# Kernel tuning notes

Measured on AMD Instinct MI355X. Metric: run time of the kernel, lower is better.

## Reference

```python
import jax, jax.numpy as jnp
import numpy as np

B, T, N, D, H = 16, 96, 325, 64, 64
BS = 1e-09  # bias init constant

def _xavier(key, shape):
    fan_in, fan_out = shape
    limit = float(np.sqrt(6.0 / (fan_in + fan_out)))
    return jax.random.uniform(key, shape, jnp.float32, -limit, limit)

def setup_inputs() -> dict:
    key = jax.random.key(0)
    k = jax.random.split(key, 6)
    return {
        "x": jax.random.normal(k[0], (B, T, N, D), jnp.float32),
        "o_s": jax.random.normal(k[1], (B, T, N, D), jnp.float32),
        "U_x": _xavier(k[2], (D, 4 * H)),
        "V_x": _xavier(k[3], (H, 4 * H)),
        "b_x": jnp.full((4 * H,), BS, jnp.float32),
        "U_g": _xavier(k[4], (D, 2 * H)),
        "V_g": _xavier(k[5], (H, 2 * H)),
        "b_g": jnp.full((2 * H,), BS, jnp.float32),
    }

def reference(x, o_s, U_x, V_x, b_x, U_g, V_g, b_g):
    b, t, n, d = x.shape
    h = V_x.shape[0]
    ht0 = jnp.zeros((b, n, h), x.dtype)
    ct0 = jnp.zeros((b, n, h), x.dtype)

    def step(carry, inp):
        ht, ct = carry
        xt, ost = inp  # [b, n, d] each
        gates = xt @ U_x + ht @ V_x + b_x          # [b, n, 4h]
        gov = jax.nn.sigmoid(ost @ U_g + ht @ V_g + b_g)  # [b, n, 2h]
        ft = jax.nn.sigmoid(gates[..., :h])
        it = jax.nn.sigmoid(gates[..., h:2 * h])
        ot = jax.nn.sigmoid(gates[..., 2 * h:3 * h])
        ut = jax.nn.sigmoid(gates[..., 3 * h:])
        gov_f = gov[..., :h]
        gov_u = gov[..., h:]
        ct = gov_f * ft * ct + gov_u * it * ut
        ht = ot * jnp.tanh(ct)
        return (ht, ct), ht

    xs = (jnp.swapaxes(x, 0, 1), jnp.swapaxes(o_s, 0, 1))  # time-major [t, b, n, d]
    (ht, ct), hseq = jax.lax.scan(step, (ht0, ct0), xs)
    hidden_seq = jnp.swapaxes(hseq, 0, 1)  # [b, t, n, h]
    return hidden_seq, ht, ct
```

## Files before the change

### kernel.cpp

```cpp
#include <hip/hip_runtime.h>
#include <stdint.h>


#define TT 96
#define NNROW 325
#define STEP_OFS 20800
#define HT_OFS 31948800
#define CT_OFS 32281600

typedef __attribute__((ext_vector_type(8))) short short8;
typedef __attribute__((ext_vector_type(4))) short short4v;
typedef __attribute__((ext_vector_type(4))) float f32x4;

#define A_STRIDE 200
#define G_STRIDE 20

#define BAR() asm volatile("s_waitcnt lgkmcnt(0)\n\ts_barrier" ::: "memory")

__device__ __forceinline__ short f2bf(float f) {
    union { float f; uint32_t u; } v; v.f = f;
    uint32_t r = (v.u + 0x7FFFu + ((v.u >> 16) & 1u)) >> 16;
    return (short)(r & 0xFFFFu);
}
__device__ __forceinline__ float frcp(float x) { return __builtin_amdgcn_rcpf(x); }
__device__ __forceinline__ float fsig(float x) { return frcp(1.0f + __expf(-x)); }
__device__ __forceinline__ float ftanh_fast(float x) {
    return 1.0f - 2.0f * frcp(__expf(2.0f * x) + 1.0f);
}

__global__ __launch_bounds__(256, 2)
void glstm_kernel(const float* __restrict__ x,
                  const float* __restrict__ o_s,
                  const float* __restrict__ U_x,
                  const float* __restrict__ V_x,
                  const float* __restrict__ b_x,
                  const float* __restrict__ U_g,
                  const float* __restrict__ V_g,
                  const float* __restrict__ b_g,
                  float* __restrict__ out)
{
    __shared__ __align__(16) short Abuf[16 * A_STRIDE];
    __shared__ __align__(16) float Gbuf[384 * G_STRIDE];

    const int tid  = threadIdx.x;
    const int g    = blockIdx.x;
    const int lane = tid & 63;
    const int w    = tid >> 6;
    const int q    = lane >> 4;
    const int ln   = lane & 15;

    short8 frW[4][4];
    short8 frG[2][4];
    #pragma unroll
    for (int nt = 0; nt < 4; ++nt) {
        const int col = w * 64 + nt * 16 + ln;
        #pragma unroll
        for (int kb = 0; kb < 4; ++kb) {
            const float* Wp = (kb < 2) ? (U_x + (size_t)(kb * 32 + q * 8) * 256 + col)
                                       : (V_x + (size_t)((kb - 2) * 32 + q * 8) * 256 + col);
            short8 fr;
            #pragma unroll
            for (int j = 0; j < 8; ++j) fr[j] = f2bf(Wp[(size_t)j * 256]);
            frW[nt][kb] = fr;
        }
    }
    #pragma unroll
    for (int nt = 0; nt < 2; ++nt) {
        const int col = w * 32 + nt * 16 + ln;
        #pragma unroll
        for (int kb = 0; kb < 4; ++kb) {
            const float* Wp = (kb < 2) ? (U_g + (size_t)(kb * 32 + q * 8) * 128 + col)
                                       : (V_g + (size_t)((kb - 2) * 32 + q * 8) * 128 + col);
            short8 fr;
            #pragma unroll
            for (int j = 0; j < 8; ++j) fr[j] = f2bf(Wp[(size_t)j * 128]);
            frG[nt][kb] = fr;
        }
    }

    const int sm = tid >> 4;
    const int sd = tid & 15;
    const int srow = g * 16 + sm;
    const int sb = srow / NNROW;
    const int sn = srow - sb * NNROW;
    const size_t sbase = ((size_t)(sb * TT) * NNROW + sn) * 64 + sd * 4;

    const int hcol = tid & 63;
    const int rg   = tid >> 6;
    float ct[4] = {0.f, 0.f, 0.f, 0.f};
    const float bf_ = b_x[hcol];
    const float bi_ = b_x[64 + hcol];
    const float bo_ = b_x[128 + hcol];
    const float bu_ = b_x[192 + hcol];
    const float bgf = b_g[hcol];
    const float bgu = b_g[64 + hcol];
    size_t obase[4];
    int    fo[4];
    #pragma unroll
    for (int e = 0; e < 4; ++e) {
        const int m = rg * 4 + e;
        const int row = g * 16 + m;
        const int b = row / NNROW;
        const int n = row - b * NNROW;
        obase[e] = ((size_t)(b * TT) * NNROW + n) * 64 + hcol;
        fo[e]    = (b * NNROW + n) * 64 + hcol;
    }

    {
        short4v z = {0, 0, 0, 0};
        *(short4v*)&Abuf[sm * A_STRIDE + 128 + sd * 4] = z;
    }

    float4 xqA = *(const float4*)(x   + sbase);
    float4 oqA = *(const float4*)(o_s + sbase);
    float4 xqB = *(const float4*)(x   + sbase + (size_t)STEP_OFS);
    float4 oqB = *(const float4*)(o_s + sbase + (size_t)STEP_OFS);

    auto step = [&](int t, float4& xq, float4& oq) {
        {
            short4v sx = { f2bf(xq.x), f2bf(xq.y), f2bf(xq.z), f2bf(xq.w) };
            short4v so = { f2bf(oq.x), f2bf(oq.y), f2bf(oq.z), f2bf(oq.w) };
            *(short4v*)&Abuf[sm * A_STRIDE + sd * 4]      = sx;
            *(short4v*)&Abuf[sm * A_STRIDE + 64 + sd * 4] = so;
        }
        {
            int tn = t + 2; if (tn > TT - 1) tn = TT - 1;
            xq = *(const float4*)(x   + sbase + (size_t)tn * STEP_OFS);
            oq = *(const float4*)(o_s + sbase + (size_t)tn * STEP_OFS);
        }
        BAR();

        {
            const short* Ab = &Abuf[ln * A_STRIDE + q * 8];
            const short8 ax0 = *(const short8*)(Ab + 0);
            const short8 ax1 = *(const short8*)(Ab + 32);
            const short8 ao0 = *(const short8*)(Ab + 64);
            const short8 ao1 = *(const short8*)(Ab + 96);
            const short8 ah0 = *(const short8*)(Ab + 128);
            const short8 ah1 = *(const short8*)(Ab + 160);
            #pragma unroll
            for (int nt = 0; nt < 4; ++nt) {
                f32x4 acc = {0.f, 0.f, 0.f, 0.f};
                acc = __builtin_amdgcn_mfma_f32_16x16x32_bf16(ax0, frW[nt][0], acc, 0, 0, 0);
                acc = __builtin_amdgcn_mfma_f32_16x16x32_bf16(ax1, frW[nt][1], acc, 0, 0, 0);
                acc = __builtin_amdgcn_mfma_f32_16x16x32_bf16(ah0, frW[nt][2], acc, 0, 0, 0);
                acc = __builtin_amdgcn_mfma_f32_16x16x32_bf16(ah1, frW[nt][3], acc, 0, 0, 0);
                const int col = w * 64 + nt * 16 + ln;
                *(f32x4*)&Gbuf[col * G_STRIDE + q * 4] = acc;
            }
            #pragma unroll
            for (int nt = 0; nt < 2; ++nt) {
                f32x4 acc = {0.f, 0.f, 0.f, 0.f};
                acc = __builtin_amdgcn_mfma_f32_16x16x32_bf16(ao0, frG[nt][0], acc, 0, 0, 0);
                acc = __builtin_amdgcn_mfma_f32_16x16x32_bf16(ao1, frG[nt][1], acc, 0, 0, 0);
                acc = __builtin_amdgcn_mfma_f32_16x16x32_bf16(ah0, frG[nt][2], acc, 0, 0, 0);
                acc = __builtin_amdgcn_mfma_f32_16x16x32_bf16(ah1, frG[nt][3], acc, 0, 0, 0);
                const int col = 256 + w * 32 + nt * 16 + ln;
                *(f32x4*)&Gbuf[col * G_STRIDE + q * 4] = acc;
            }
        }
        BAR();

        {
            const f32x4 vf = *(const f32x4*)&Gbuf[(hcol      ) * G_STRIDE + rg * 4];
            const f32x4 vi = *(const f32x4*)&Gbuf[( 64 + hcol) * G_STRIDE + rg * 4];
            const f32x4 vo = *(const f32x4*)&Gbuf[(128 + hcol) * G_STRIDE + rg * 4];
            const f32x4 vu = *(const f32x4*)&Gbuf[(192 + hcol) * G_STRIDE + rg * 4];
            const f32x4 vgf = *(const f32x4*)&Gbuf[(256 + hcol) * G_STRIDE + rg * 4];
            const f32x4 vgu = *(const f32x4*)&Gbuf[(320 + hcol) * G_STRIDE + rg * 4];
            const size_t tofs = (size_t)t * STEP_OFS;
            #pragma unroll
            for (int e = 0; e < 4; ++e) {
                const int m = rg * 4 + e;
                float c = fsig(vgf[e] + bgf) * fsig(vf[e] + bf_) * ct[e]
                        + fsig(vgu[e] + bgu) * fsig(vi[e] + bi_) * fsig(vu[e] + bu_);
                ct[e] = c;
                float h = fsig(vo[e] + bo_) * ftanh_fast(c);
                out[obase[e] + tofs] = h;
                Abuf[m * A_STRIDE + 128 + hcol] = f2bf(h);
                if (t == TT - 1) {
                    out[HT_OFS + fo[e]] = h;
                    out[CT_OFS + fo[e]] = c;
                }
            }
        }
    };

    for (int t = 0; t < TT; t += 2) {
        step(t,     xqA, oqA);
        step(t + 1, xqB, oqB);
    }
}

extern "C" void kernel_launch(void* const* d_in, const int* in_sizes, int n_in,
                              void* d_out, int out_size, void* d_ws, size_t ws_size,
                              hipStream_t stream) {
    const float* x   = (const float*)d_in[0];
    const float* o_s = (const float*)d_in[1];
    const float* U_x = (const float*)d_in[2];
    const float* V_x = (const float*)d_in[3];
    const float* b_x = (const float*)d_in[4];
    const float* V_g = (const float*)d_in[6];
    const float* U_g = (const float*)d_in[5];
    const float* b_g = (const float*)d_in[7];
    float* out = (float*)d_out;

    glstm_kernel<<<dim3(325), dim3(256), 0, stream>>>(x, o_s, U_x, V_x, b_x, U_g, V_g, b_g, out);
}
```

Baseline: 366.4 us.

## Remap MFMA gate tiles per wave to drop LDS gate exchange and barrier

Each wave now computes the f/i/o/u and gov gate tiles for the same 16 hidden channels, so the pointwise LSTM update runs directly on the MFMA accumulators. The Gbuf round-trip and one of the two barriers per timestep go away. X/O/H staging becomes double-buffered, XOR-swizzled LDS tiles, and the prefetch distance grows by one step. The activations are rewritten with exp2 and shared reciprocals, and bf16 conversion uses v_cvt_pk_bf16_f32, which may shift rounding and numerics slightly.

```diff
diff --git a/kernel.cpp b/kernel.cpp
--- a/kernel.cpp
+++ b/kernel.cpp
@@ -9,11 +9,7 @@
 #define CT_OFS 32281600
 
 typedef __attribute__((ext_vector_type(8))) short short8;
-typedef __attribute__((ext_vector_type(4))) short short4v;
 typedef __attribute__((ext_vector_type(4))) float f32x4;
-
-#define A_STRIDE 200
-#define G_STRIDE 20
 
 #define BAR() asm volatile("s_waitcnt lgkmcnt(0)\n\ts_barrier" ::: "memory")
 
@@ -23,9 +19,11 @@
     return (short)(r & 0xFFFFu);
 }
 __device__ __forceinline__ float frcp(float x) { return __builtin_amdgcn_rcpf(x); }
-__device__ __forceinline__ float fsig(float x) { return frcp(1.0f + __expf(-x)); }
-__device__ __forceinline__ float ftanh_fast(float x) {
-    return 1.0f - 2.0f * frcp(__expf(2.0f * x) + 1.0f);
+__device__ __forceinline__ float ex2(float x)  { return __builtin_amdgcn_exp2f(x); }
+__device__ __forceinline__ uint32_t cvtpk(float lo, float hi) {
+    uint32_t r;
+    asm("v_cvt_pk_bf16_f32 %0, %1, %2" : "=v"(r) : "v"(lo), "v"(hi));
+    return r;
 }
 
 __global__ __launch_bounds__(256, 2)
@@ -39,8 +37,9 @@
                   const float* __restrict__ b_g,
                   float* __restrict__ out)
 {
-    __shared__ __align__(16) short Abuf[16 * A_STRIDE];
-    __shared__ __align__(16) float Gbuf[384 * G_STRIDE];
+    __shared__ __align__(16) short Xb[2][1024];
+    __shared__ __align__(16) short Ob[2][1024];
+    __shared__ __align__(16) short Hb[2][1024];
 
     const int tid  = threadIdx.x;
     const int g    = blockIdx.x;
@@ -49,32 +48,35 @@
     const int q    = lane >> 4;
     const int ln   = lane & 15;
 
-    short8 frW[4][4];
-    short8 frG[2][4];
+    short8 fWx[4][2], fWh[4][2], fGo[2][2], fGh[2][2];
     #pragma unroll
-    for (int nt = 0; nt < 4; ++nt) {
-        const int col = w * 64 + nt * 16 + ln;
-        #pragma unroll
-        for (int kb = 0; kb < 4; ++kb) {
-            const float* Wp = (kb < 2) ? (U_x + (size_t)(kb * 32 + q * 8) * 256 + col)
-                                       : (V_x + (size_t)((kb - 2) * 32 + q * 8) * 256 + col);
-            short8 fr;
+    for (int gt = 0; gt < 4; ++gt) {
+        const int col = gt * 64 + w * 16 + ln;
+        #pragma unroll
+        for (int kb = 0; kb < 2; ++kb) {
+            short8 a, b;
             #pragma unroll
-            for (int j = 0; j < 8; ++j) fr[j] = f2bf(Wp[(size_t)j * 256]);
-            frW[nt][kb] = fr;
+            for (int j = 0; j < 8; ++j) {
+                const int row = kb * 32 + q * 8 + j;
+                a[j] = f2bf(U_x[(size_t)row * 256 + col]);
+                b[j] = f2bf(V_x[(size_t)row * 256 + col]);
+            }
+            fWx[gt][kb] = a; fWh[gt][kb] = b;
         }
     }
     #pragma unroll
-    for (int nt = 0; nt < 2; ++nt) {
-        const int col = w * 32 + nt * 16 + ln;
-        #pragma unroll
-        for (int kb = 0; kb < 4; ++kb) {
-            const float* Wp = (kb < 2) ? (U_g + (size_t)(kb * 32 + q * 8) * 128 + col)
-                                       : (V_g + (size_t)((kb - 2) * 32 + q * 8) * 128 + col);
-            short8 fr;
+    for (int gt = 0; gt < 2; ++gt) {
+        const int col = gt * 64 + w * 16 + ln;
+        #pragma unroll
+        for (int kb = 0; kb < 2; ++kb) {
+            short8 a, b;
             #pragma unroll
-            for (int j = 0; j < 8; ++j) fr[j] = f2bf(Wp[(size_t)j * 128]);
-            frG[nt][kb] = fr;
+            for (int j = 0; j < 8; ++j) {
+                const int row = kb * 32 + q * 8 + j;
+                a[j] = f2bf(U_g[(size_t)row * 128 + col]);
+                b[j] = f2bf(V_g[(size_t)row * 128 + col]);
+            }
+            fGo[gt][kb] = a; fGh[gt][kb] = b;
         }
     }
 
@@ -84,106 +86,130 @@
     const int sb = srow / NNROW;
     const int sn = srow - sb * NNROW;
     const size_t sbase = ((size_t)(sb * TT) * NNROW + sn) * 64 + sd * 4;
-
-    const int hcol = tid & 63;
-    const int rg   = tid >> 6;
-    float ct[4] = {0.f, 0.f, 0.f, 0.f};
-    const float bf_ = b_x[hcol];
-    const float bi_ = b_x[64 + hcol];
-    const float bo_ = b_x[128 + hcol];
-    const float bu_ = b_x[192 + hcol];
-    const float bgf = b_g[hcol];
-    const float bgu = b_g[64 + hcol];
+    const int stofs = (sm * 64 + (((sd >> 1) ^ (sm & 7)) << 3) + (sd & 1) * 4) * 2;
+
+    const int o0 = ln * 128 + (((q    ) ^ (ln & 7)) << 4);
+    const int o1 = ln * 128 + (((4 + q) ^ (ln & 7)) << 4);
+
+    const int ch = w * 16 + ln;
+    const float NL2E = -1.44269504f;
+    const float nbf  = NL2E * b_x[ch];
+    const float nbi  = NL2E * b_x[64  + ch];
+    const float nbo  = NL2E * b_x[128 + ch];
+    const float nbu  = NL2E * b_x[192 + ch];
+    const float nbgf = NL2E * b_g[ch];
+    const float nbgu = NL2E * b_g[64 + ch];
+
     size_t obase[4];
     int    fo[4];
+    int    hofs[4];
     #pragma unroll
     for (int e = 0; e < 4; ++e) {
-        const int m = rg * 4 + e;
+        const int m = q * 4 + e;
         const int row = g * 16 + m;
         const int b = row / NNROW;
         const int n = row - b * NNROW;
-        obase[e] = ((size_t)(b * TT) * NNROW + n) * 64 + hcol;
-        fo[e]    = (b * NNROW + n) * 64 + hcol;
-    }
+        obase[e] = ((size_t)(b * TT) * NNROW + n) * 64 + ch;
+        fo[e]    = (b * NNROW + n) * 64 + ch;
+        hofs[e]  = m * 64 + ((((ch >> 3) ^ (m & 7)) << 3) | (ch & 7));
+    }
+    float ct4[4] = {0.f, 0.f, 0.f, 0.f};
 
     {
-        short4v z = {0, 0, 0, 0};
-        *(short4v*)&Abuf[sm * A_STRIDE + 128 + sd * 4] = z;
-    }
-
-    float4 xqA = *(const float4*)(x   + sbase);
-    float4 oqA = *(const float4*)(o_s + sbase);
-    float4 xqB = *(const float4*)(x   + sbase + (size_t)STEP_OFS);
-    float4 oqB = *(const float4*)(o_s + sbase + (size_t)STEP_OFS);
+        float4 x0 = *(const float4*)(x   + sbase);
+        float4 s0 = *(const float4*)(o_s + sbase);
+        uint2 sx; sx.x = cvtpk(x0.x, x0.y); sx.y = cvtpk(x0.z, x0.w);
+        uint2 so; so.x = cvtpk(s0.x, s0.y); so.y = cvtpk(s0.z, s0.w);
+        *(uint2*)((char*)&Xb[0][0] + stofs) = sx;
+        *(uint2*)((char*)&Ob[0][0] + stofs) = so;
+        uint2 z; z.x = 0u; z.y = 0u;
+        *(uint2*)((char*)&Hb[0][0] + tid * 8) = z;
+    }
+    float4 xqA = *(const float4*)(x   + sbase + 1 * (size_t)STEP_OFS);
+    float4 oqA = *(const float4*)(o_s + sbase + 1 * (size_t)STEP_OFS);
+    float4 xqB = *(const float4*)(x   + sbase + 2 * (size_t)STEP_OFS);
+    float4 oqB = *(const float4*)(o_s + sbase + 2 * (size_t)STEP_OFS);
+    BAR();
 
     auto step = [&](int t, float4& xq, float4& oq) {
+        const int p  = t & 1;
+        const int pn = p ^ 1;
+        const char* xb = (const char*)&Xb[p][0];
+        const char* ob = (const char*)&Ob[p][0];
+        const char* hb = (const char*)&Hb[p][0];
+        const short8 ax0 = *(const short8*)(xb + o0);
+        const short8 ax1 = *(const short8*)(xb + o1);
+        const short8 ao0 = *(const short8*)(ob + o0);
+        const short8 ao1 = *(const short8*)(ob + o1);
+        const short8 ah0 = *(const short8*)(hb + o0);
+        const short8 ah1 = *(const short8*)(hb + o1);
+
+        f32x4 aF[4], aG[2];
+        #pragma unroll
+        for (int gt = 0; gt < 4; ++gt) {
+            f32x4 acc = {0.f, 0.f, 0.f, 0.f};
+            acc = __builtin_amdgcn_mfma_f32_16x16x32_bf16(ax0, fWx[gt][0], acc, 0, 0, 0);
+            acc = __builtin_amdgcn_mfma_f32_16x16x32_bf16(ax1, fWx[gt][1], acc, 0, 0, 0);
+            acc = __builtin_amdgcn_mfma_f32_16x16x32_bf16(ah0, fWh[gt][0], acc, 0, 0, 0);
+            acc = __builtin_amdgcn_mfma_f32_16x16x32_bf16(ah1, fWh[gt][1], acc, 0, 0, 0);
+            aF[gt] = acc;
+        }
+        #pragma unroll
+        for (int gt = 0; gt < 2; ++gt) {
+            f32x4 acc = {0.f, 0.f, 0.f, 0.f};
+            acc = __builtin_amdgcn_mfma_f32_16x16x32_bf16(ao0, fGo[gt][0], acc, 0, 0, 0);
+            acc = __builtin_amdgcn_mfma_f32_16x16x32_bf16(ao1, fGo[gt][1], acc, 0, 0, 0);
+            acc = __builtin_amdgcn_mfma_f32_16x16x32_bf16(ah0, fGh[gt][0], acc, 0, 0, 0);
+            acc = __builtin_amdgcn_mfma_f32_16x16x32_bf16(ah1, fGh[gt][1], acc, 0, 0, 0);
+            aG[gt] = acc;
+        }
+
         {
-            short4v sx = { f2bf(xq.x), f2bf(xq.y), f2bf(xq.z), f2bf(xq.w) };
-            short4v so = { f2bf(oq.x), f2bf(oq.y), f2bf(oq.z), f2bf(oq.w) };
-            *(short4v*)&Abuf[sm * A_STRIDE + sd * 4]      = sx;
-            *(short4v*)&Abuf[sm * A_STRIDE + 64 + sd * 4] = so;
-        }
-        {
-            int tn = t + 2; if (tn > TT - 1) tn = TT - 1;
+            uint2 sx; sx.x = cvtpk(xq.x, xq.y); sx.y = cvtpk(xq.z, xq.w);
+            uint2 so; so.x = cvtpk(oq.x, oq.y); so.y = cvtpk(oq.z, oq.w);
+            *(uint2*)((char*)&Xb[pn][0] + stofs) = sx;
+            *(uint2*)((char*)&Ob[pn][0] + stofs) = so;
+            int tn = t + 3; if (tn > TT - 1) tn = TT - 1;
             xq = *(const float4*)(x   + sbase + (size_t)tn * STEP_OFS);
             oq = *(const float4*)(o_s + sbase + (size_t)tn * STEP_OFS);
         }
+
+        const size_t tofs = (size_t)t * STEP_OFS;
+        float hv[4];
+        #pragma unroll
+        for (int e = 0; e < 4; ++e) {
+            float ef  = ex2(fmaf(aF[0][e], NL2E, nbf));
+            float ei  = ex2(fmaf(aF[1][e], NL2E, nbi));
+            float eo  = ex2(fmaf(aF[2][e], NL2E, nbo));
+            float eu  = ex2(fmaf(aF[3][e], NL2E, nbu));
+            float egf = ex2(fmaf(aG[0][e], NL2E, nbgf));
+            float egu = ex2(fmaf(aG[1][e], NL2E, nbgu));
+            float rf = frcp((1.f + ef) * (1.f + egf));
+            float ru = frcp(((1.f + ei) * (1.f + eu)) * (1.f + egu));
+            float c  = fmaf(ct4[e], rf, ru);
+            ct4[e] = c;
+            float E  = ex2(c * 2.88539008f);
+            float th = fmaf(-2.f, frcp(E + 1.f), 1.f);
+            float h  = th * frcp(1.f + eo);
+            hv[e] = h;
+            out[obase[e] + tofs] = h;
+            if (t == TT - 1) {
+                out[HT_OFS + fo[e]] = h;
+                out[CT_OFS + fo[e]] = c;
+            }
+        }
+
+        {
+            union { uint32_t u; short s[2]; } h01, h23;
+            h01.u = cvtpk(hv[0], hv[1]);
+            h23.u = cvtpk(hv[2], hv[3]);
+            short* hn = &Hb[pn][0];
+            hn[hofs[0]] = h01.s[0];
+            hn[hofs[1]] = h01.s[1];
+            hn[hofs[2]] = h23.s[0];
+            hn[hofs[3]] = h23.s[1];
+        }
         BAR();
-
-        {
-            const short* Ab = &Abuf[ln * A_STRIDE + q * 8];
-            const short8 ax0 = *(const short8*)(Ab + 0);
-            const short8 ax1 = *(const short8*)(Ab + 32);
-            const short8 ao0 = *(const short8*)(Ab + 64);
-            const short8 ao1 = *(const short8*)(Ab + 96);
-            const short8 ah0 = *(const short8*)(Ab + 128);
-            const short8 ah1 = *(const short8*)(Ab + 160);
-            #pragma unroll
-            for (int nt = 0; nt < 4; ++nt) {
-                f32x4 acc = {0.f, 0.f, 0.f, 0.f};
-                acc = __builtin_amdgcn_mfma_f32_16x16x32_bf16(ax0, frW[nt][0], acc, 0, 0, 0);
-                acc = __builtin_amdgcn_mfma_f32_16x16x32_bf16(ax1, frW[nt][1], acc, 0, 0, 0);
-                acc = __builtin_amdgcn_mfma_f32_16x16x32_bf16(ah0, frW[nt][2], acc, 0, 0, 0);
-                acc = __builtin_amdgcn_mfma_f32_16x16x32_bf16(ah1, frW[nt][3], acc, 0, 0, 0);
-                const int col = w * 64 + nt * 16 + ln;
-                *(f32x4*)&Gbuf[col * G_STRIDE + q * 4] = acc;
-            }
-            #pragma unroll
-            for (int nt = 0; nt < 2; ++nt) {
-                f32x4 acc = {0.f, 0.f, 0.f, 0.f};
-                acc = __builtin_amdgcn_mfma_f32_16x16x32_bf16(ao0, frG[nt][0], acc, 0, 0, 0);
-                acc = __builtin_amdgcn_mfma_f32_16x16x32_bf16(ao1, frG[nt][1], acc, 0, 0, 0);
-                acc = __builtin_amdgcn_mfma_f32_16x16x32_bf16(ah0, frG[nt][2], acc, 0, 0, 0);
-                acc = __builtin_amdgcn_mfma_f32_16x16x32_bf16(ah1, frG[nt][3], acc, 0, 0, 0);
-                const int col = 256 + w * 32 + nt * 16 + ln;
-                *(f32x4*)&Gbuf[col * G_STRIDE + q * 4] = acc;
-            }
-        }
-        BAR();
-
-        {
-            const f32x4 vf = *(const f32x4*)&Gbuf[(hcol      ) * G_STRIDE + rg * 4];
-            const f32x4 vi = *(const f32x4*)&Gbuf[( 64 + hcol) * G_STRIDE + rg * 4];
-            const f32x4 vo = *(const f32x4*)&Gbuf[(128 + hcol) * G_STRIDE + rg * 4];
-            const f32x4 vu = *(const f32x4*)&Gbuf[(192 + hcol) * G_STRIDE + rg * 4];
-            const f32x4 vgf = *(const f32x4*)&Gbuf[(256 + hcol) * G_STRIDE + rg * 4];
-            const f32x4 vgu = *(const f32x4*)&Gbuf[(320 + hcol) * G_STRIDE + rg * 4];
-            const size_t tofs = (size_t)t * STEP_OFS;
-            #pragma unroll
-            for (int e = 0; e < 4; ++e) {
-                const int m = rg * 4 + e;
-                float c = fsig(vgf[e] + bgf) * fsig(vf[e] + bf_) * ct[e]
-                        + fsig(vgu[e] + bgu) * fsig(vi[e] + bi_) * fsig(vu[e] + bu_);
-                ct[e] = c;
-                float h = fsig(vo[e] + bo_) * ftanh_fast(c);
-                out[obase[e] + tofs] = h;
-                Abuf[m * A_STRIDE + 128 + hcol] = f2bf(h);
-                if (t == TT - 1) {
-                    out[HT_OFS + fo[e]] = h;
-                    out[CT_OFS + fo[e]] = c;
-                }
-            }
-        }
     };
 
     for (int t = 0; t < TT; t += 2) {
@@ -200,8 +226,8 @@
     const float* U_x = (const float*)d_in[2];
     const float* V_x = (const float*)d_in[3];
     const float* b_x = (const float*)d_in[4];
+    const float* U_g = (const float*)d_in[5];
     const float* V_g = (const float*)d_in[6];
-    const float* U_g = (const float*)d_in[5];
     const float* b_g = (const float*)d_in[7];
     float* out = (float*)d_out;
 
```

After: 344.1 us. -6.1%, faster.
